# Kernel optimization log

Measured on AMD Instinct MI355X. Metric: run time of the kernel, lower is better.

## Reference

```python
import jax, jax.numpy as jnp
import numpy as np

B, N, K, H = 2, 2048, 48, 128
NIN = 2 * H          # num_in = 2*num_hidden (ProteinMPNN wiring)
FF = 4 * H           # PositionWiseFeedForward hidden
SCALE = 30.0
EPS = 1e-5           # torch LayerNorm default eps


def _ln(x, g, b):
    m = jnp.mean(x, axis=-1, keepdims=True)
    v = jnp.mean((x - m) ** 2, axis=-1, keepdims=True)
    return (x - m) / jnp.sqrt(v + EPS) * g + b


def _gelu(x):
    return jax.nn.gelu(x, approximate=False)  # torch.nn.GELU default (erf)


def _lin(x, W, b):
    return x @ W + b


def setup_inputs() -> dict:
    key = jax.random.key(0)
    ks = jax.random.split(key, 24)
    s = 0.05
    inp = {
        "h_V": jax.random.normal(ks[0], (B, N, H), jnp.float32),
        "h_E": jax.random.normal(ks[1], (B, N, K, H), jnp.float32),
        "E_idx": jax.random.randint(ks[2], (B, N, K), 0, N, jnp.int64),
        "mask_V": jnp.ones((B, N), jnp.float32),
        "mask_attend": jnp.ones((B, N, K), jnp.float32),
        # message MLP (node update): W1 in = H + NIN = 3H
        "W1": jax.random.normal(ks[3], (3 * H, H), jnp.float32) * s,
        "b1": jnp.zeros((H,), jnp.float32),
        "W2": jax.random.normal(ks[4], (H, H), jnp.float32) * s,
        "b2": jnp.zeros((H,), jnp.float32),
        "W3": jax.random.normal(ks[5], (H, H), jnp.float32) * s,
        "b3": jnp.zeros((H,), jnp.float32),
        # PositionWiseFeedForward
        "Wd_in": jax.random.normal(ks[6], (H, FF), jnp.float32) * s,
        "bd_in": jnp.zeros((FF,), jnp.float32),
        "Wd_out": jax.random.normal(ks[7], (FF, H), jnp.float32) * s,
        "bd_out": jnp.zeros((H,), jnp.float32),
        # edge-update MLP: W11 in = H + NIN = 3H
        "W11": jax.random.normal(ks[8], (3 * H, H), jnp.float32) * s,
        "b11": jnp.zeros((H,), jnp.float32),
        "W12": jax.random.normal(ks[9], (H, H), jnp.float32) * s,
        "b12": jnp.zeros((H,), jnp.float32),
        "W13": jax.random.normal(ks[10], (H, H), jnp.float32) * s,
        "b13": jnp.zeros((H,), jnp.float32),
        # LayerNorms
        "n1g": jnp.ones((H,), jnp.float32), "n1b": jnp.zeros((H,), jnp.float32),
        "n2g": jnp.ones((H,), jnp.float32), "n2b": jnp.zeros((H,), jnp.float32),
        "n3g": jnp.ones((H,), jnp.float32), "n3b": jnp.zeros((H,), jnp.float32),
    }
    return inp


def reference(h_V, h_E, E_idx, mask_V, mask_attend,
              W1, b1, W2, b2, W3, b3,
              Wd_in, bd_in, Wd_out, bd_out,
              W11, b11, W12, b12, W13, b13,
              n1g, n1b, n2g, n2b, n3g, n3b):
    gather = jax.vmap(lambda hv, idx: hv[idx])  # [B,N,H],[B,N,K] -> [B,N,K,H]

    # --- node update: cat_neighbors_nodes + expand + 3-layer GELU MLP ---
    h_nb = gather(h_V, E_idx)                                   # [B,N,K,H]
    hV_exp = jnp.broadcast_to(h_V[:, :, None, :], h_nb.shape)   # [B,N,K,H]
    h_EV = jnp.concatenate([hV_exp, h_E, h_nb], axis=-1)        # [B,N,K,3H]
    h_msg = _lin(_gelu(_lin(_gelu(_lin(h_EV, W1, b1)), W2, b2)), W3, b3)
    h_msg = mask_attend[..., None] * h_msg
    dh = jnp.sum(h_msg, axis=-2) / SCALE                        # masked-sum reduce
    h_V = _ln(h_V + dh, n1g, n1b)

    # --- position-wise FFN ---
    dh = _lin(_gelu(_lin(h_V, Wd_in, bd_in)), Wd_out, bd_out)
    h_V = _ln(h_V + dh, n2g, n2b)
    h_V = mask_V[..., None] * h_V

    # --- edge update (not last layer) ---
    h_nb2 = gather(h_V, E_idx)
    hV_exp2 = jnp.broadcast_to(h_V[:, :, None, :], h_nb2.shape)
    h_EV2 = jnp.concatenate([hV_exp2, h_E, h_nb2], axis=-1)     # [B,N,K,3H]
    h_msg2 = _lin(_gelu(_lin(_gelu(_lin(h_EV2, W11, b11)), W12, b12)), W13, b13)
    h_E = _ln(h_E + h_msg2, n3g, n3b)
    return (h_V, h_E)
```

## Files before the change

kernel.cpp:

```cpp
#include <hip/hip_runtime.h>
#include <hip/hip_bf16.h>
#include <stdint.h>

#define XP2 264
#define MP 136
#define FFP 520
#define EPIP 132

typedef __attribute__((ext_vector_type(8))) short bf16x8;
typedef __attribute__((ext_vector_type(4))) float f32x4;

__device__ __forceinline__ f32x4 mfma16(bf16x8 a, bf16x8 b, f32x4 c) {
  return __builtin_amdgcn_mfma_f32_16x16x32_bf16(a, b, c, 0, 0, 0);
}

__device__ __forceinline__ uint16_t f2b(float f) {
  union { __hip_bfloat16 h; uint16_t u; } v;
  v.h = __float2bfloat16(f);
  return v.u;
}
__device__ __forceinline__ uint32_t pk2f(float a, float b) {
  union { __hip_bfloat162 h; uint32_t u; } v;
  v.h = __float22bfloat162_rn(make_float2(a, b));
  return v.u;
}
__device__ __forceinline__ float gelu_f(float x) {
  float u = __builtin_fmaf(x * x, 0.044715f, 1.0f);
  float e = __builtin_amdgcn_exp2f(-2.302585093f * x * u);
  return x * __builtin_amdgcn_rcpf(1.0f + e);
}

__global__ __launch_bounds__(256) void k_prep(
    const float* __restrict__ hV,
    const float* __restrict__ W1, const float* __restrict__ W2, const float* __restrict__ W3,
    const float* __restrict__ WdIn, const float* __restrict__ WdOut,
    const float* __restrict__ W11, const float* __restrict__ W12, const float* __restrict__ W13,
    uint16_t* __restrict__ hVb,
    uint16_t* __restrict__ W1t, uint16_t* __restrict__ W2t, uint16_t* __restrict__ W3t,
    uint16_t* __restrict__ WdInT, uint16_t* __restrict__ WdOutT,
    uint16_t* __restrict__ W11t, uint16_t* __restrict__ W12t, uint16_t* __restrict__ W13t) {
  int i = blockIdx.x * 256 + threadIdx.x;
  if (i < 524288) { hVb[i] = f2b(hV[i]); return; }
  int j = i - 524288;
  if (j < 49152) { int n = j / 384, k = j - n * 384; W1t[j] = f2b(W1[k * 128 + n]); return; }
  j -= 49152;
  if (j < 16384) { int n = j >> 7, k = j & 127; W2t[j] = f2b(W2[k * 128 + n]); return; }
  j -= 16384;
  if (j < 16384) { int n = j >> 7, k = j & 127; W3t[j] = f2b(W3[k * 128 + n]); return; }
  j -= 16384;
  if (j < 65536) { int n = j >> 7, k = j & 127; WdInT[j] = f2b(WdIn[k * 512 + n]); return; }
  j -= 65536;
  if (j < 65536) { int n = j >> 9, k = j & 511; WdOutT[j] = f2b(WdOut[k * 128 + n]); return; }
  j -= 65536;
  if (j < 49152) { int n = j / 384, k = j - n * 384; W11t[j] = f2b(W11[k * 128 + n]); return; }
  j -= 49152;
  if (j < 16384) { int n = j >> 7, k = j & 127; W12t[j] = f2b(W12[k * 128 + n]); return; }
  j -= 16384;
  if (j < 16384) { int n = j >> 7, k = j & 127; W13t[j] = f2b(W13[k * 128 + n]); return; }
}

__global__ __launch_bounds__(256) void k_vec(
    const uint16_t* __restrict__ Xb, const uint16_t* __restrict__ Wt,
    const float* __restrict__ bias, float* __restrict__ C) {
  const int tid = threadIdx.x;
  const int lane = tid & 63, w = tid >> 6, l15 = lane & 15, lg = lane >> 4;
  const int row0 = blockIdx.x * 64 + w * 16;
  f32x4 acc[8] = {};
#pragma unroll
  for (int ks = 0; ks < 4; ++ks) {
    bf16x8 a = *(const bf16x8*)(Xb + (row0 + l15) * 128 + ks * 32 + lg * 8);
#pragma unroll
    for (int j = 0; j < 8; ++j) {
      bf16x8 bb = *(const bf16x8*)(Wt + (j * 16 + l15) * 384 + ks * 32 + lg * 8);
      acc[j] = mfma16(a, bb, acc[j]);
    }
  }
#pragma unroll
  for (int j = 0; j < 8; ++j) {
    float bs = bias[j * 16 + l15];
#pragma unroll
    for (int r = 0; r < 4; ++r)
      C[(row0 + lg * 4 + r) * 128 + j * 16 + l15] = acc[j][r] + bs;
  }
}

#define STAGE_LOAD(TB, GSRC)                                                        \
  do {                                                                              \
    if (cc < 16) {                                                                  \
      _Pragma("unroll") for (int it = 0; it < 6; ++it) {                            \
        const float* s_ = hE + (size_t)((TB) + kr0 + it * 8) * 128 + cc * 8;        \
        sA[it] = *(const float4*)s_;                                                \
        sB[it] = *(const float4*)(s_ + 4);                                          \
      }                                                                             \
    } else {                                                                        \
      _Pragma("unroll") for (int it = 0; it < 6; ++it) {                            \
        int e_ = (TB) + kr0 + it * 8;                                               \
        int nb_ = ((e_ >= 98304) ? 2048 : 0) + eidx[e_];                            \
        *(uint4*)&sA[it] = *(const uint4*)((GSRC) + (size_t)nb_ * 128 + (cc - 16) * 8); \
      }                                                                             \
    }                                                                               \
  } while (0)

#define STAGE_WRITE(BUF)                                                            \
  do {                                                                              \
    if (cc < 16) {                                                                  \
      _Pragma("unroll") for (int it = 0; it < 6; ++it) {                            \
        uint4 v_ = make_uint4(pk2f(sA[it].x, sA[it].y), pk2f(sA[it].z, sA[it].w),   \
                              pk2f(sB[it].x, sB[it].y), pk2f(sB[it].z, sB[it].w));  \
        *(uint4*)((BUF) + (kr0 + it * 8) * XP2 + cc * 8) = v_;                      \
      }                                                                             \
    } else {                                                                        \
      _Pragma("unroll") for (int it = 0; it < 6; ++it)                              \
        *(uint4*)((BUF) + (kr0 + it * 8) * XP2 + cc * 8) = *(uint4*)&sA[it];        \
    }                                                                               \
  } while (0)

#define LAYER256(WT, XSRC, ACC)                                                     \
  do {                                                                              \
    const uint16_t* wr0_ = (WT) + (w * 32 + l15) * 384 + 128 + lg * 8;              \
    const uint16_t* wr1_ = wr0_ + 16 * 384;                                         \
    _Pragma("unroll 2") for (int ks = 0; ks < 8; ++ks) {                            \
      bf16x8 bA_ = *(const bf16x8*)(wr0_ + ks * 32);                                \
      bf16x8 bB_ = *(const bf16x8*)(wr1_ + ks * 32);                                \
      _Pragma("unroll") for (int m = 0; m < 3; ++m) {                               \
        bf16x8 a_ = *(const bf16x8*)((XSRC) + (m * 16 + l15) * XP2 + ks * 32 + lg * 8); \
        ACC[m][0] = mfma16(a_, bA_, ACC[m][0]);                                     \
        ACC[m][1] = mfma16(a_, bB_, ACC[m][1]);                                     \
      }                                                                             \
    }                                                                               \
  } while (0)

#define LAYER128(WT, ASRC, ACC)                                                     \
  do {                                                                              \
    const uint16_t* wr0_ = (WT) + (w * 32 + l15) * 128 + lg * 8;                    \
    const uint16_t* wr1_ = wr0_ + 16 * 128;                                         \
    _Pragma("unroll") for (int ks = 0; ks < 4; ++ks) {                              \
      bf16x8 bA_ = *(const bf16x8*)(wr0_ + ks * 32);                                \
      bf16x8 bB_ = *(const bf16x8*)(wr1_ + ks * 32);                                \
      _Pragma("unroll") for (int m = 0; m < 3; ++m) {                               \
        bf16x8 a_ = *(const bf16x8*)((ASRC) + (m * 16 + l15) * MP + ks * 32 + lg * 8); \
        ACC[m][0] = mfma16(a_, bA_, ACC[m][0]);                                     \
        ACC[m][1] = mfma16(a_, bB_, ACC[m][1]);                                     \
      }                                                                              \
    }                                                                               \
  } while (0)

#define GSTORE(ACC, BIAS, DST)                                                      \
  do {                                                                              \
    float bA_ = (BIAS)[w * 32 + l15];                                               \
    float bB_ = (BIAS)[w * 32 + 16 + l15];                                          \
    _Pragma("unroll") for (int m = 0; m < 3; ++m)                                   \
    _Pragma("unroll") for (int r = 0; r < 4; ++r) {                                 \
      int row_ = m * 16 + lg * 4 + r;                                               \
      (DST)[row_ * MP + w * 32 + l15] = f2b(gelu_f(ACC[m][0][r] + bA_));            \
      (DST)[row_ * MP + w * 32 + 16 + l15] = f2b(gelu_f(ACC[m][1][r] + bB_));       \
    }                                                                               \
  } while (0)

#define GSTORE0(ACC, DST)                                                           \
  do {                                                                              \
    _Pragma("unroll") for (int m = 0; m < 3; ++m)                                   \
    _Pragma("unroll") for (int r = 0; r < 4; ++r) {                                 \
      int row_ = m * 16 + lg * 4 + r;                                               \
      (DST)[row_ * MP + w * 32 + l15] = f2b(gelu_f(ACC[m][0][r]));                  \
      (DST)[row_ * MP + w * 32 + 16 + l15] = f2b(gelu_f(ACC[m][1][r]));             \
    }                                                                               \
  } while (0)

#define ACC_INIT(ACC, CV, ND)                                                       \
  do {                                                                              \
    float c0_ = (CV)[(size_t)(ND) * 128 + w * 32 + l15];                            \
    float c1_ = (CV)[(size_t)(ND) * 128 + w * 32 + 16 + l15];                       \
    _Pragma("unroll") for (int m = 0; m < 3; ++m) {                                 \
      ACC[m][0] = (f32x4){c0_, c0_, c0_, c0_};                                      \
      ACC[m][1] = (f32x4){c1_, c1_, c1_, c1_};                                      \
    }                                                                               \
  } while (0)

__global__ __launch_bounds__(256, 2) void k_node(
    const float* __restrict__ hV, const float* __restrict__ hE,
    const int* __restrict__ eidx, const float* __restrict__ maskA,
    const float* __restrict__ bias2, const float* __restrict__ bias3,
    const float* __restrict__ g1, const float* __restrict__ be1,
    const uint16_t* __restrict__ hVb, const float* __restrict__ C1,
    const uint16_t* __restrict__ W1t, const uint16_t* __restrict__ W2t,
    const uint16_t* __restrict__ W3t,
    float* __restrict__ hV1, uint16_t* __restrict__ hV1b) {
  __shared__ __align__(16) unsigned char lds[76800];
  uint16_t* xtA = (uint16_t*)lds;
  uint16_t* xtB = (uint16_t*)(lds + 25344);
  uint16_t* midA = (uint16_t*)(lds + 50688);
  uint16_t* midB = (uint16_t*)(lds + 63744);
  float* dh = (float*)(lds + 50688);

  const int tid = threadIdx.x;
  const int lane = tid & 63;
  const int w = tid >> 6;
  const int l15 = lane & 15;
  const int lg = lane >> 4;
  const int kr0 = tid >> 5;
  const int cc = tid & 31;

  float4 sA[6], sB[6];
  uint16_t* xc = xtA;
  uint16_t* xn = xtB;

  {
    int tile0 = blockIdx.x;
    STAGE_LOAD(tile0 * 48, hVb);
    STAGE_WRITE(xc);
  }

  for (int t = 0; t < 8; ++t) {
    const int tile = t * 512 + blockIdx.x;
    const int nd = tile;
    const int tbase = tile * 48;
    __syncthreads();

    if (t < 7) STAGE_LOAD((tile + 512) * 48, hVb);

    f32x4 acc1[3][2];
    ACC_INIT(acc1, C1, nd);
    LAYER256(W1t, xc, acc1);
    __syncthreads();
    GSTORE0(acc1, midA);
    __syncthreads();

    f32x4 acc2[3][2] = {};
    LAYER128(W2t, midA, acc2);
    GSTORE(acc2, bias2, midB);
    __syncthreads();

    f32x4 acc3[3][2] = {};
    LAYER128(W3t, midB, acc3);

    if (t < 7) STAGE_WRITE(xn);

    {
      float bA = bias3[w * 32 + l15];
      float bB = bias3[w * 32 + 16 + l15];
      float s0 = 0.f, s1 = 0.f;
#pragma unroll
      for (int m = 0; m < 3; ++m)
#pragma unroll
        for (int r = 0; r < 4; ++r) {
          int row = m * 16 + lg * 4 + r;
          float mk = maskA[tbase + row];
          s0 += (acc3[m][0][r] + bA) * mk;
          s1 += (acc3[m][1][r] + bB) * mk;
        }
      s0 += __shfl_xor(s0, 16); s0 += __shfl_xor(s0, 32);
      s1 += __shfl_xor(s1, 16); s1 += __shfl_xor(s1, 32);
      if (lg == 0) { dh[w * 32 + l15] = s0; dh[w * 32 + 16 + l15] = s1; }
    }
    __syncthreads();

    if (w == 0) {
      const float inv = 1.0f / 30.0f;
      float x0 = hV[(size_t)nd * 128 + lane] + dh[lane] * inv;
      float x1 = hV[(size_t)nd * 128 + 64 + lane] + dh[64 + lane] * inv;
      float s = x0 + x1, q = x0 * x0 + x1 * x1;
#pragma unroll
      for (int off = 1; off < 64; off <<= 1) {
        s += __shfl_xor(s, off);
        q += __shfl_xor(q, off);
      }
      float mean = s * (1.0f / 128.0f);
      float var = q * (1.0f / 128.0f) - mean * mean;
      float rstd = rsqrtf(var + 1e-5f);
      float y0 = (x0 - mean) * rstd * g1[lane] + be1[lane];
      float y1 = (x1 - mean) * rstd * g1[64 + lane] + be1[64 + lane];
      hV1[(size_t)nd * 128 + lane] = y0;
      hV1[(size_t)nd * 128 + 64 + lane] = y1;
      hV1b[(size_t)nd * 128 + lane] = f2b(y0);
      hV1b[(size_t)nd * 128 + 64 + lane] = f2b(y1);
    }

    uint16_t* tmp = xc; xc = xn; xn = tmp;
  }
}

__global__ __launch_bounds__(256, 2) void k_ffn(
    const float* __restrict__ hV1, const uint16_t* __restrict__ hV1b,
    const float* __restrict__ maskV,
    const float* __restrict__ bdin, const float* __restrict__ bdout,
    const float* __restrict__ g2, const float* __restrict__ be2,
    const uint16_t* __restrict__ WdInT, const uint16_t* __restrict__ WdOutT,
    float* __restrict__ outV, uint16_t* __restrict__ hV2b) {
  __shared__ __align__(16) unsigned char lds[20992];
  uint16_t* xa = (uint16_t*)lds;
  uint16_t* mf = (uint16_t*)(lds + 4352);
  float* epi = (float*)(lds + 4352);

  const int tid = threadIdx.x;
  const int lane = tid & 63;
  const int w = tid >> 6;
  const int l15 = lane & 15;
  const int lg = lane >> 4;
  const int node0 = blockIdx.x * 16;

  {
    int row = tid >> 4, c = tid & 15;
    *(uint4*)(xa + row * 136 + (c << 3)) =
        *(const uint4*)(hV1b + (node0 + row) * 128 + (c << 3));
  }
  __syncthreads();

  f32x4 acc[8] = {};
  {
    const uint16_t* ar = xa + l15 * 136 + lg * 8;
#pragma unroll
    for (int ks = 0; ks < 4; ++ks) {
      bf16x8 a = *(const bf16x8*)(ar + ks * 32);
#pragma unroll
      for (int j = 0; j < 8; ++j) {
        bf16x8 bb = *(const bf16x8*)(WdInT + ((w * 8 + j) * 16 + l15) * 128 + ks * 32 + lg * 8);
        acc[j] = mfma16(a, bb, acc[j]);
      }
    }
  }
#pragma unroll
  for (int j = 0; j < 8; ++j) {
    int col = (w * 8 + j) * 16 + l15;
    float bs = bdin[col];
#pragma unroll
    for (int r = 0; r < 4; ++r) {
      int row = lg * 4 + r;
      mf[row * FFP + col] = f2b(gelu_f(acc[j][r] + bs));
    }
  }
  __syncthreads();

  f32x4 acc2[2] = {};
  {
    const uint16_t* mr = mf + l15 * FFP + lg * 8;
#pragma unroll 4
    for (int ks = 0; ks < 16; ++ks) {
      bf16x8 a = *(const bf16x8*)(mr + ks * 32);
#pragma unroll
      for (int t = 0; t < 2; ++t) {
        bf16x8 bb = *(const bf16x8*)(WdOutT + ((w * 2 + t) * 16 + l15) * 512 + ks * 32 + lg * 8);
        acc2[t] = mfma16(a, bb, acc2[t]);
      }
    }
  }
  __syncthreads();
#pragma unroll
  for (int t = 0; t < 2; ++t) {
    int col = (w * 2 + t) * 16 + l15;
    float bs = bdout[col];
#pragma unroll
    for (int r = 0; r < 4; ++r) {
      int row = lg * 4 + r;
      epi[row * EPIP + col] = acc2[t][r] + bs;
    }
  }
  __syncthreads();

#pragma unroll
  for (int rr = 0; rr < 4; ++rr) {
    int row = w * 4 + rr;
    int node = node0 + row;
    float x0 = epi[row * EPIP + lane] + hV1[node * 128 + lane];
    float x1 = epi[row * EPIP + 64 + lane] + hV1[node * 128 + 64 + lane];
    float s = x0 + x1, q = x0 * x0 + x1 * x1;
#pragma unroll
    for (int off = 1; off < 64; off <<= 1) {
      s += __shfl_xor(s, off);
      q += __shfl_xor(q, off);
    }
    float mean = s * (1.0f / 128.0f);
    float var = q * (1.0f / 128.0f) - mean * mean;
    float rstd = rsqrtf(var + 1e-5f);
    float mv = maskV[node];
    float y0 = mv * ((x0 - mean) * rstd * g2[lane] + be2[lane]);
    float y1 = mv * ((x1 - mean) * rstd * g2[64 + lane] + be2[64 + lane]);
    outV[node * 128 + lane] = y0;
    outV[node * 128 + 64 + lane] = y1;
    hV2b[node * 128 + lane] = f2b(y0);
    hV2b[node * 128 + 64 + lane] = f2b(y1);
  }
}

__global__ __launch_bounds__(256, 2) void k_edge(
    const float* __restrict__ hE, const int* __restrict__ eidx,
    const float* __restrict__ bias2, const float* __restrict__ bias3,
    const float* __restrict__ g3, const float* __restrict__ be3,
    const uint16_t* __restrict__ hV2b, const float* __restrict__ C2,
    const uint16_t* __restrict__ W1t, const uint16_t* __restrict__ W2t,
    const uint16_t* __restrict__ W3t,
    float* __restrict__ outE) {
  __shared__ __align__(16) unsigned char lds[76800];
  uint16_t* xtA = (uint16_t*)lds;
  uint16_t* xtB = (uint16_t*)(lds + 25344);
  uint16_t* midA = (uint16_t*)(lds + 50688);
  uint16_t* midB = (uint16_t*)(lds + 63744);
  float* part_s = (float*)(lds + 50688);
  float* part_q = (float*)(lds + 51456);
  float* mstd = (float*)(lds + 52224);

  const int tid = threadIdx.x;
  const int lane = tid & 63;
  const int w = tid >> 6;
  const int l15 = lane & 15;
  const int lg = lane >> 4;
  const int kr0 = tid >> 5;
  const int cc = tid & 31;

  float4 sA[6], sB[6];
  uint16_t* xc = xtA;
  uint16_t* xn = xtB;

  {
    int tile0 = blockIdx.x;
    STAGE_LOAD(tile0 * 48, hV2b);
    STAGE_WRITE(xc);
  }

  for (int t = 0; t < 8; ++t) {
    const int tile = t * 512 + blockIdx.x;
    const int nd = tile;
    const int tbase = tile * 48;
    __syncthreads();

    if (t < 7) STAGE_LOAD((tile + 512) * 48, hV2b);

    f32x4 acc1[3][2];
    ACC_INIT(acc1, C2, nd);
    LAYER256(W1t, xc, acc1);
    __syncthreads();
    GSTORE0(acc1, midA);
    __syncthreads();

    f32x4 acc2[3][2] = {};
    LAYER128(W2t, midA, acc2);
    GSTORE(acc2, bias2, midB);
    __syncthreads();

    f32x4 acc3[3][2] = {};
    LAYER128(W3t, midB, acc3);

    if (t < 7) STAGE_WRITE(xn);

    const float bA = bias3[w * 32 + l15];
    const float bB = bias3[w * 32 + 16 + l15];

    float xs0[3][4], xs1[3][4];
#pragma unroll
    for (int m = 0; m < 3; ++m)
#pragma unroll
      for (int r = 0; r < 4; ++r) {
        int row = m * 16 + lg * 4 + r;
        size_t e = (size_t)tbase + row;
        xs0[m][r] = acc3[m][0][r] + bA + hE[e * 128 + w * 32 + l15];
        xs1[m][r] = acc3[m][1][r] + bB + hE[e * 128 + w * 32 + 16 + l15];
        float s = xs0[m][r] + xs1[m][r];
        float q = xs0[m][r] * xs0[m][r] + xs1[m][r] * xs1[m][r];
        s += __shfl_xor(s, 1); q += __shfl_xor(q, 1);
        s += __shfl_xor(s, 2); q += __shfl_xor(q, 2);
        s += __shfl_xor(s, 4); q += __shfl_xor(q, 4);
        s += __shfl_xor(s, 8); q += __shfl_xor(q, 8);
        if (l15 == 0) { part_s[row * 4 + w] = s; part_q[row * 4 + w] = q; }
      }
    __syncthreads();

    if (tid < 48) {
      float s = part_s[tid * 4] + part_s[tid * 4 + 1] + part_s[tid * 4 + 2] + part_s[tid * 4 + 3];
      float q = part_q[tid * 4] + part_q[tid * 4 + 1] + part_q[tid * 4 + 2] + part_q[tid * 4 + 3];
      float mean = s * (1.0f / 128.0f);
      float var = q * (1.0f / 128.0f) - mean * mean;
      mstd[tid * 2] = mean;
      mstd[tid * 2 + 1] = rsqrtf(var + 1e-5f);
    }
    __syncthreads();

    const float gA = g3[w * 32 + l15], beA = be3[w * 32 + l15];
    const float gB = g3[w * 32 + 16 + l15], beB = be3[w * 32 + 16 + l15];
#pragma unroll
    for (int m = 0; m < 3; ++m)
#pragma unroll
      for (int r = 0; r < 4; ++r) {
        int row = m * 16 + lg * 4 + r;
        size_t e = (size_t)tbase + row;
        float mean = mstd[row * 2];
        float rstd = mstd[row * 2 + 1];
        outE[e * 128 + w * 32 + l15] = (xs0[m][r] - mean) * rstd * gA + beA;
        outE[e * 128 + w * 32 + 16 + l15] = (xs1[m][r] - mean) * rstd * gB + beB;
      }

    uint16_t* tmp = xc; xc = xn; xn = tmp;
  }
}

extern "C" void kernel_launch(void* const* d_in, const int* in_sizes, int n_in,
                              void* d_out, int out_size, void* d_ws, size_t ws_size,
                              hipStream_t stream) {
  const float* hV = (const float*)d_in[0];
  const float* hE = (const float*)d_in[1];
  const int* eidx = (const int*)d_in[2];
  const float* maskV = (const float*)d_in[3];
  const float* maskA = (const float*)d_in[4];
  const float* W1 = (const float*)d_in[5];   const float* b1 = (const float*)d_in[6];
  const float* W2 = (const float*)d_in[7];   const float* b2 = (const float*)d_in[8];
  const float* W3 = (const float*)d_in[9];   const float* b3 = (const float*)d_in[10];
  const float* WdIn = (const float*)d_in[11];  const float* bdin = (const float*)d_in[12];
  const float* WdOut = (const float*)d_in[13]; const float* bdout = (const float*)d_in[14];
  const float* W11 = (const float*)d_in[15]; const float* b11 = (const float*)d_in[16];
  const float* W12 = (const float*)d_in[17]; const float* b12 = (const float*)d_in[18];
  const float* W13 = (const float*)d_in[19]; const float* b13 = (const float*)d_in[20];
  const float* n1g = (const float*)d_in[21]; const float* n1b = (const float*)d_in[22];
  const float* n2g = (const float*)d_in[23]; const float* n2b = (const float*)d_in[24];
  const float* n3g = (const float*)d_in[25]; const float* n3b = (const float*)d_in[26];

  char* ws = (char*)d_ws;
  uint16_t* hVb    = (uint16_t*)(ws + 0);
  uint16_t* W1t    = (uint16_t*)(ws + 1048576);
  uint16_t* W2t    = (uint16_t*)(ws + 1146880);
  uint16_t* W3t    = (uint16_t*)(ws + 1179648);
  uint16_t* WdInT  = (uint16_t*)(ws + 1212416);
  uint16_t* WdOutT = (uint16_t*)(ws + 1343488);
  uint16_t* W11t   = (uint16_t*)(ws + 1474560);
  uint16_t* W12t   = (uint16_t*)(ws + 1572864);
  uint16_t* W13t   = (uint16_t*)(ws + 1605632);
  float*    hV1    = (float*)(ws + 1638400);
  uint16_t* hV1b   = (uint16_t*)(ws + 3735552);
  uint16_t* hV2b   = (uint16_t*)(ws + 4784128);
  float*    C1     = (float*)(ws + 5832704);
  float*    C2     = (float*)(ws + 7929856);

  float* outV = (float*)d_out;
  float* outE = (float*)d_out + 524288;

  k_prep<<<3200, 256, 0, stream>>>(hV, W1, W2, W3, WdIn, WdOut, W11, W12, W13,
                                   hVb, W1t, W2t, W3t, WdInT, WdOutT, W11t, W12t, W13t);
  k_vec<<<64, 256, 0, stream>>>(hVb, W1t, b1, C1);
  k_node<<<512, 256, 0, stream>>>(hV, hE, eidx, maskA, b2, b3, n1g, n1b,
                                  hVb, C1, W1t, W2t, W3t, hV1, hV1b);
  k_ffn<<<256, 256, 0, stream>>>(hV1, hV1b, maskV, bdin, bdout, n2g, n2b,
                                 WdInT, WdOutT, outV, hV2b);
  k_vec<<<64, 256, 0, stream>>>(hV2b, W11t, b11, C2);
  k_edge<<<512, 256, 0, stream>>>(hE, eidx, b12, b13, n3g, n3b,
                                  hV2b, C2, W11t, W12t, W13t, outE);
}
```

Measured before the change: 234.0 us.

## Shrink LDS footprint and retile edge kernel to 32-row tiles for occupancy

Splits the staged input into separate edge and gathered-neighbour LDS buffers and collapses the two mid buffers into one, reusing it with extra barriers, so both kernels use less LDS. The edge kernel moves from 48-row to 32-row tiles with 768 blocks and launch bounds allowing 3 blocks per CU. Because a 32-row tile no longer maps to one node, the per-row node bias is gathered with a divide-by-48 trick. The residual h_E is now read from the bf16 LDS copy instead of fp32 global memory, which saves global traffic but adds bf16 rounding error to the edge output.

```diff
diff --git a/kernel.cpp b/kernel.cpp
--- a/kernel.cpp
+++ b/kernel.cpp
@@ -2,7 +2,6 @@
 #include <hip/hip_bf16.h>
 #include <stdint.h>
 
-#define XP2 264
 #define MP 136
 #define FFP 520
 #define EPIP 132
@@ -19,6 +18,10 @@
   v.h = __float2bfloat16(f);
   return v.u;
 }
+__device__ __forceinline__ float b2f(uint16_t h) {
+  union { uint32_t u; float f; } v; v.u = ((uint32_t)h) << 16;
+  return v.f;
+}
 __device__ __forceinline__ uint32_t pk2f(float a, float b) {
   union { __hip_bfloat162 h; uint32_t u; } v;
   v.h = __float22bfloat162_rn(make_float2(a, b));
@@ -28,6 +31,9 @@
   float u = __builtin_fmaf(x * x, 0.044715f, 1.0f);
   float e = __builtin_amdgcn_exp2f(-2.302585093f * x * u);
   return x * __builtin_amdgcn_rcpf(1.0f + e);
+}
+__device__ __forceinline__ int div48(int e) {
+  return (int)((((unsigned)e >> 4) * 0xAAABu) >> 17);
 }
 
 __global__ __launch_bounds__(256) void k_prep(
@@ -84,60 +90,31 @@
   }
 }
 
-#define STAGE_LOAD(TB, GSRC)                                                        \
-  do {                                                                              \
-    if (cc < 16) {                                                                  \
-      _Pragma("unroll") for (int it = 0; it < 6; ++it) {                            \
-        const float* s_ = hE + (size_t)((TB) + kr0 + it * 8) * 128 + cc * 8;        \
-        sA[it] = *(const float4*)s_;                                                \
-        sB[it] = *(const float4*)(s_ + 4);                                          \
-      }                                                                             \
-    } else {                                                                        \
-      _Pragma("unroll") for (int it = 0; it < 6; ++it) {                            \
-        int e_ = (TB) + kr0 + it * 8;                                               \
-        int nb_ = ((e_ >= 98304) ? 2048 : 0) + eidx[e_];                            \
-        *(uint4*)&sA[it] = *(const uint4*)((GSRC) + (size_t)nb_ * 128 + (cc - 16) * 8); \
-      }                                                                             \
-    }                                                                               \
-  } while (0)
-
-#define STAGE_WRITE(BUF)                                                            \
-  do {                                                                              \
-    if (cc < 16) {                                                                  \
-      _Pragma("unroll") for (int it = 0; it < 6; ++it) {                            \
-        uint4 v_ = make_uint4(pk2f(sA[it].x, sA[it].y), pk2f(sA[it].z, sA[it].w),   \
-                              pk2f(sB[it].x, sB[it].y), pk2f(sB[it].z, sB[it].w));  \
-        *(uint4*)((BUF) + (kr0 + it * 8) * XP2 + cc * 8) = v_;                      \
-      }                                                                             \
-    } else {                                                                        \
-      _Pragma("unroll") for (int it = 0; it < 6; ++it)                              \
-        *(uint4*)((BUF) + (kr0 + it * 8) * XP2 + cc * 8) = *(uint4*)&sA[it];        \
-    }                                                                               \
-  } while (0)
-
-#define LAYER256(WT, XSRC, ACC)                                                     \
+#define LAYER256S(WT, XE, XG, ACC, MM)                                              \
   do {                                                                              \
     const uint16_t* wr0_ = (WT) + (w * 32 + l15) * 384 + 128 + lg * 8;              \
     const uint16_t* wr1_ = wr0_ + 16 * 384;                                         \
-    _Pragma("unroll 2") for (int ks = 0; ks < 8; ++ks) {                            \
+    _Pragma("unroll") for (int ks = 0; ks < 8; ++ks) {                              \
+      const uint16_t* xb_ = (ks < 4) ? (XE) : (XG);                                 \
+      int kk_ = ks & 3;                                                             \
       bf16x8 bA_ = *(const bf16x8*)(wr0_ + ks * 32);                                \
       bf16x8 bB_ = *(const bf16x8*)(wr1_ + ks * 32);                                \
-      _Pragma("unroll") for (int m = 0; m < 3; ++m) {                               \
-        bf16x8 a_ = *(const bf16x8*)((XSRC) + (m * 16 + l15) * XP2 + ks * 32 + lg * 8); \
+      _Pragma("unroll") for (int m = 0; m < (MM); ++m) {                            \
+        bf16x8 a_ = *(const bf16x8*)(xb_ + (m * 16 + l15) * MP + kk_ * 32 + lg * 8);\
         ACC[m][0] = mfma16(a_, bA_, ACC[m][0]);                                     \
         ACC[m][1] = mfma16(a_, bB_, ACC[m][1]);                                     \
       }                                                                             \
     }                                                                               \
   } while (0)
 
-#define LAYER128(WT, ASRC, ACC)                                                     \
+#define LAYER128S(WT, ASRC, ACC, MM)                                                \
   do {                                                                              \
     const uint16_t* wr0_ = (WT) + (w * 32 + l15) * 128 + lg * 8;                    \
     const uint16_t* wr1_ = wr0_ + 16 * 128;                                         \
     _Pragma("unroll") for (int ks = 0; ks < 4; ++ks) {                              \
       bf16x8 bA_ = *(const bf16x8*)(wr0_ + ks * 32);                                \
       bf16x8 bB_ = *(const bf16x8*)(wr1_ + ks * 32);                                \
-      _Pragma("unroll") for (int m = 0; m < 3; ++m) {                               \
+      _Pragma("unroll") for (int m = 0; m < (MM); ++m) {                            \
         bf16x8 a_ = *(const bf16x8*)((ASRC) + (m * 16 + l15) * MP + ks * 32 + lg * 8); \
         ACC[m][0] = mfma16(a_, bA_, ACC[m][0]);                                     \
         ACC[m][1] = mfma16(a_, bB_, ACC[m][1]);                                     \
@@ -145,11 +122,11 @@
     }                                                                               \
   } while (0)
 
-#define GSTORE(ACC, BIAS, DST)                                                      \
+#define GSTOREM(ACC, BIAS, DST, MM)                                                 \
   do {                                                                              \
     float bA_ = (BIAS)[w * 32 + l15];                                               \
     float bB_ = (BIAS)[w * 32 + 16 + l15];                                          \
-    _Pragma("unroll") for (int m = 0; m < 3; ++m)                                   \
+    _Pragma("unroll") for (int m = 0; m < (MM); ++m)                                \
     _Pragma("unroll") for (int r = 0; r < 4; ++r) {                                 \
       int row_ = m * 16 + lg * 4 + r;                                               \
       (DST)[row_ * MP + w * 32 + l15] = f2b(gelu_f(ACC[m][0][r] + bA_));            \
@@ -157,23 +134,13 @@
     }                                                                               \
   } while (0)
 
-#define GSTORE0(ACC, DST)                                                           \
+#define GSTORE0M(ACC, DST, MM)                                                      \
   do {                                                                              \
-    _Pragma("unroll") for (int m = 0; m < 3; ++m)                                   \
+    _Pragma("unroll") for (int m = 0; m < (MM); ++m)                                \
     _Pragma("unroll") for (int r = 0; r < 4; ++r) {                                 \
       int row_ = m * 16 + lg * 4 + r;                                               \
       (DST)[row_ * MP + w * 32 + l15] = f2b(gelu_f(ACC[m][0][r]));                  \
       (DST)[row_ * MP + w * 32 + 16 + l15] = f2b(gelu_f(ACC[m][1][r]));             \
-    }                                                                               \
-  } while (0)
-
-#define ACC_INIT(ACC, CV, ND)                                                       \
-  do {                                                                              \
-    float c0_ = (CV)[(size_t)(ND) * 128 + w * 32 + l15];                            \
-    float c1_ = (CV)[(size_t)(ND) * 128 + w * 32 + 16 + l15];                       \
-    _Pragma("unroll") for (int m = 0; m < 3; ++m) {                                 \
-      ACC[m][0] = (f32x4){c0_, c0_, c0_, c0_};                                      \
-      ACC[m][1] = (f32x4){c1_, c1_, c1_, c1_};                                      \
     }                                                                               \
   } while (0)
 
@@ -186,55 +153,79 @@
     const uint16_t* __restrict__ W1t, const uint16_t* __restrict__ W2t,
     const uint16_t* __restrict__ W3t,
     float* __restrict__ hV1, uint16_t* __restrict__ hV1b) {
-  __shared__ __align__(16) unsigned char lds[76800];
-  uint16_t* xtA = (uint16_t*)lds;
-  uint16_t* xtB = (uint16_t*)(lds + 25344);
-  uint16_t* midA = (uint16_t*)(lds + 50688);
-  uint16_t* midB = (uint16_t*)(lds + 63744);
-  float* dh = (float*)(lds + 50688);
+  __shared__ __align__(16) unsigned char lds[65792];
+  uint16_t* xE0 = (uint16_t*)lds;
+  uint16_t* xE1 = (uint16_t*)(lds + 13056);
+  uint16_t* xG0 = (uint16_t*)(lds + 26112);
+  uint16_t* xG1 = (uint16_t*)(lds + 39168);
+  uint16_t* mid = (uint16_t*)(lds + 52224);
+  float* dh = (float*)(lds + 65280);
 
   const int tid = threadIdx.x;
   const int lane = tid & 63;
   const int w = tid >> 6;
   const int l15 = lane & 15;
   const int lg = lane >> 4;
-  const int kr0 = tid >> 5;
-  const int cc = tid & 31;
-
-  float4 sA[6], sB[6];
-  uint16_t* xc = xtA;
-  uint16_t* xn = xtB;
-
-  {
-    int tile0 = blockIdx.x;
-    STAGE_LOAD(tile0 * 48, hVb);
-    STAGE_WRITE(xc);
-  }
+
+  float4 fE[6];
+  uint4 gV[3];
+
+#define NLOAD48(TB)                                                                 \
+  _Pragma("unroll") for (int i_ = 0; i_ < 3; ++i_) {                                \
+    int c_ = tid + i_ * 256, row_ = c_ >> 4, p_ = c_ & 15;                          \
+    const float* sE_ = hE + (size_t)((TB) + row_) * 128 + p_ * 8;                   \
+    fE[i_ * 2] = *(const float4*)sE_;                                               \
+    fE[i_ * 2 + 1] = *(const float4*)(sE_ + 4);                                     \
+    int e_ = (TB) + row_;                                                           \
+    int nb_ = ((e_ >= 98304) ? 2048 : 0) + eidx[e_];                                \
+    gV[i_] = *(const uint4*)(hVb + (size_t)nb_ * 128 + p_ * 8);                     \
+  }
+
+#define NWRITE48(XE, XG)                                                            \
+  _Pragma("unroll") for (int i_ = 0; i_ < 3; ++i_) {                                \
+    int c_ = tid + i_ * 256, row_ = c_ >> 4, p_ = c_ & 15;                          \
+    uint4 v_ = make_uint4(pk2f(fE[i_ * 2].x, fE[i_ * 2].y),                         \
+                          pk2f(fE[i_ * 2].z, fE[i_ * 2].w),                         \
+                          pk2f(fE[i_ * 2 + 1].x, fE[i_ * 2 + 1].y),                 \
+                          pk2f(fE[i_ * 2 + 1].z, fE[i_ * 2 + 1].w));                \
+    *(uint4*)((XE) + row_ * MP + p_ * 8) = v_;                                      \
+    *(uint4*)((XG) + row_ * MP + p_ * 8) = gV[i_];                                  \
+  }
+
+  uint16_t *xEc = xE0, *xEn = xE1, *xGc = xG0, *xGn = xG1;
+
+  NLOAD48(blockIdx.x * 48);
+  NWRITE48(xEc, xGc);
+  __syncthreads();
 
   for (int t = 0; t < 8; ++t) {
     const int tile = t * 512 + blockIdx.x;
-    const int nd = tile;
     const int tbase = tile * 48;
-    __syncthreads();
-
-    if (t < 7) STAGE_LOAD((tile + 512) * 48, hVb);
+    if (t < 7) NLOAD48((tile + 512) * 48);
 
     f32x4 acc1[3][2];
-    ACC_INIT(acc1, C1, nd);
-    LAYER256(W1t, xc, acc1);
-    __syncthreads();
-    GSTORE0(acc1, midA);
+    {
+      float c0 = C1[(size_t)tile * 128 + w * 32 + l15];
+      float c1 = C1[(size_t)tile * 128 + w * 32 + 16 + l15];
+#pragma unroll
+      for (int m = 0; m < 3; ++m) {
+        acc1[m][0] = (f32x4){c0, c0, c0, c0};
+        acc1[m][1] = (f32x4){c1, c1, c1, c1};
+      }
+    }
+    LAYER256S(W1t, xEc, xGc, acc1, 3);
+    GSTORE0M(acc1, mid, 3);
     __syncthreads();
 
     f32x4 acc2[3][2] = {};
-    LAYER128(W2t, midA, acc2);
-    GSTORE(acc2, bias2, midB);
+    LAYER128S(W2t, mid, acc2, 3);
+    __syncthreads();
+    GSTOREM(acc2, bias2, mid, 3);
     __syncthreads();
 
     f32x4 acc3[3][2] = {};
-    LAYER128(W3t, midB, acc3);
-
-    if (t < 7) STAGE_WRITE(xn);
+    LAYER128S(W3t, mid, acc3, 3);
+    if (t < 7) NWRITE48(xEn, xGn);
 
     {
       float bA = bias3[w * 32 + l15];
@@ -257,8 +248,8 @@
 
     if (w == 0) {
       const float inv = 1.0f / 30.0f;
-      float x0 = hV[(size_t)nd * 128 + lane] + dh[lane] * inv;
-      float x1 = hV[(size_t)nd * 128 + 64 + lane] + dh[64 + lane] * inv;
+      float x0 = hV[(size_t)tile * 128 + lane] + dh[lane] * inv;
+      float x1 = hV[(size_t)tile * 128 + 64 + lane] + dh[64 + lane] * inv;
       float s = x0 + x1, q = x0 * x0 + x1 * x1;
 #pragma unroll
       for (int off = 1; off < 64; off <<= 1) {
@@ -270,14 +261,19 @@
       float rstd = rsqrtf(var + 1e-5f);
       float y0 = (x0 - mean) * rstd * g1[lane] + be1[lane];
       float y1 = (x1 - mean) * rstd * g1[64 + lane] + be1[64 + lane];
-      hV1[(size_t)nd * 128 + lane] = y0;
-      hV1[(size_t)nd * 128 + 64 + lane] = y1;
-      hV1b[(size_t)nd * 128 + lane] = f2b(y0);
-      hV1b[(size_t)nd * 128 + 64 + lane] = f2b(y1);
-    }
-
-    uint16_t* tmp = xc; xc = xn; xn = tmp;
-  }
+      hV1[(size_t)tile * 128 + lane] = y0;
+      hV1[(size_t)tile * 128 + 64 + lane] = y1;
+      hV1b[(size_t)tile * 128 + lane] = f2b(y0);
+      hV1b[(size_t)tile * 128 + 64 + lane] = f2b(y1);
+    }
+    __syncthreads();
+
+    uint16_t* tp;
+    tp = xEc; xEc = xEn; xEn = tp;
+    tp = xGc; xGc = xGn; xGn = tp;
+  }
+#undef NLOAD48
+#undef NWRITE48
 }
 
 __global__ __launch_bounds__(256, 2) void k_ffn(
@@ -382,7 +378,7 @@
   }
 }
 
-__global__ __launch_bounds__(256, 2) void k_edge(
+__global__ __launch_bounds__(256, 3) void k_edge(
     const float* __restrict__ hE, const int* __restrict__ eidx,
     const float* __restrict__ bias2, const float* __restrict__ bias3,
     const float* __restrict__ g3, const float* __restrict__ be3,
@@ -390,70 +386,98 @@
     const uint16_t* __restrict__ W1t, const uint16_t* __restrict__ W2t,
     const uint16_t* __restrict__ W3t,
     float* __restrict__ outE) {
-  __shared__ __align__(16) unsigned char lds[76800];
-  uint16_t* xtA = (uint16_t*)lds;
-  uint16_t* xtB = (uint16_t*)(lds + 25344);
-  uint16_t* midA = (uint16_t*)(lds + 50688);
-  uint16_t* midB = (uint16_t*)(lds + 63744);
-  float* part_s = (float*)(lds + 50688);
-  float* part_q = (float*)(lds + 51456);
-  float* mstd = (float*)(lds + 52224);
+  __shared__ __align__(16) unsigned char lds[44800];
+  uint16_t* xE0 = (uint16_t*)lds;
+  uint16_t* xE1 = (uint16_t*)(lds + 8704);
+  uint16_t* xG0 = (uint16_t*)(lds + 17408);
+  uint16_t* xG1 = (uint16_t*)(lds + 26112);
+  uint16_t* mid = (uint16_t*)(lds + 34816);
+  float* part_s = (float*)(lds + 43520);
+  float* part_q = (float*)(lds + 44032);
+  float* mstd = (float*)(lds + 44544);
 
   const int tid = threadIdx.x;
   const int lane = tid & 63;
   const int w = tid >> 6;
   const int l15 = lane & 15;
   const int lg = lane >> 4;
-  const int kr0 = tid >> 5;
-  const int cc = tid & 31;
-
-  float4 sA[6], sB[6];
-  uint16_t* xc = xtA;
-  uint16_t* xn = xtB;
-
-  {
-    int tile0 = blockIdx.x;
-    STAGE_LOAD(tile0 * 48, hV2b);
-    STAGE_WRITE(xc);
-  }
+
+  float4 fA0, fA1, fA2, fA3;
+  uint4 gA0, gA1;
+
+#define ELOAD32(TB)                                                                 \
+  {                                                                                 \
+    int row_ = tid >> 3, p_ = tid & 7;                                              \
+    const float* sE_ = hE + (size_t)((TB) + row_) * 128 + p_ * 16;                  \
+    fA0 = *(const float4*)sE_;       fA1 = *(const float4*)(sE_ + 4);               \
+    fA2 = *(const float4*)(sE_ + 8); fA3 = *(const float4*)(sE_ + 12);              \
+    int e_ = (TB) + row_;                                                           \
+    int nb_ = ((e_ >= 98304) ? 2048 : 0) + eidx[e_];                                \
+    const uint16_t* sG_ = hV2b + (size_t)nb_ * 128 + p_ * 16;                       \
+    gA0 = *(const uint4*)sG_;  gA1 = *(const uint4*)(sG_ + 8);                      \
+  }
+
+#define EWRITE32(XE, XG)                                                            \
+  {                                                                                 \
+    int row_ = tid >> 3, p_ = tid & 7;                                              \
+    uint4 v0_ = make_uint4(pk2f(fA0.x, fA0.y), pk2f(fA0.z, fA0.w),                  \
+                           pk2f(fA1.x, fA1.y), pk2f(fA1.z, fA1.w));                 \
+    uint4 v1_ = make_uint4(pk2f(fA2.x, fA2.y), pk2f(fA2.z, fA2.w),                  \
+                           pk2f(fA3.x, fA3.y), pk2f(fA3.z, fA3.w));                 \
+    *(uint4*)((XE) + row_ * MP + p_ * 16) = v0_;                                    \
+    *(uint4*)((XE) + row_ * MP + p_ * 16 + 8) = v1_;                                \
+    *(uint4*)((XG) + row_ * MP + p_ * 16) = gA0;                                    \
+    *(uint4*)((XG) + row_ * MP + p_ * 16 + 8) = gA1;                                \
+  }
+
+  uint16_t *xEc = xE0, *xEn = xE1, *xGc = xG0, *xGn = xG1;
+
+  ELOAD32(blockIdx.x * 32);
+  EWRITE32(xEc, xGc);
+  __syncthreads();
 
   for (int t = 0; t < 8; ++t) {
-    const int tile = t * 512 + blockIdx.x;
-    const int nd = tile;
-    const int tbase = tile * 48;
-    __syncthreads();
-
-    if (t < 7) STAGE_LOAD((tile + 512) * 48, hV2b);
-
-    f32x4 acc1[3][2];
-    ACC_INIT(acc1, C2, nd);
-    LAYER256(W1t, xc, acc1);
-    __syncthreads();
-    GSTORE0(acc1, midA);
-    __syncthreads();
-
-    f32x4 acc2[3][2] = {};
-    LAYER128(W2t, midA, acc2);
-    GSTORE(acc2, bias2, midB);
-    __syncthreads();
-
-    f32x4 acc3[3][2] = {};
-    LAYER128(W3t, midB, acc3);
-
-    if (t < 7) STAGE_WRITE(xn);
+    const int tile = t * 768 + blockIdx.x;
+    const int tbase = tile * 32;
+    if (t < 7) ELOAD32((tile + 768) * 32);
+
+    f32x4 acc1[2][2];
+#pragma unroll
+    for (int m = 0; m < 2; ++m)
+#pragma unroll
+      for (int r = 0; r < 4; ++r) {
+        int row = m * 16 + lg * 4 + r;
+        int nd = div48(tbase + row);
+        acc1[m][0][r] = C2[(size_t)nd * 128 + w * 32 + l15];
+        acc1[m][1][r] = C2[(size_t)nd * 128 + w * 32 + 16 + l15];
+      }
+    LAYER256S(W1t, xEc, xGc, acc1, 2);
+    GSTORE0M(acc1, mid, 2);
+    __syncthreads();
+
+    f32x4 acc2[2][2] = {};
+    LAYER128S(W2t, mid, acc2, 2);
+    __syncthreads();
+    GSTOREM(acc2, bias2, mid, 2);
+    __syncthreads();
+
+    f32x4 acc3[2][2] = {};
+    LAYER128S(W3t, mid, acc3, 2);
+    if (t < 7) EWRITE32(xEn, xGn);
 
     const float bA = bias3[w * 32 + l15];
     const float bB = bias3[w * 32 + 16 + l15];
 
-    float xs0[3][4], xs1[3][4];
-#pragma unroll
-    for (int m = 0; m < 3; ++m)
+    float xs0[2][4], xs1[2][4];
+#pragma unroll
+    for (int m = 0; m < 2; ++m)
 #pragma unroll
       for (int r = 0; r < 4; ++r) {
         int row = m * 16 + lg * 4 + r;
-        size_t e = (size_t)tbase + row;
-        xs0[m][r] = acc3[m][0][r] + bA + hE[e * 128 + w * 32 + l15];
-        xs1[m][r] = acc3[m][1][r] + bB + hE[e * 128 + w * 32 + 16 + l15];
+        float r0 = b2f(xEc[row * MP + w * 32 + l15]);
+        float r1 = b2f(xEc[row * MP + w * 32 + 16 + l15]);
+        xs0[m][r] = acc3[m][0][r] + bA + r0;
+        xs1[m][r] = acc3[m][1][r] + bB + r1;
         float s = xs0[m][r] + xs1[m][r];
         float q = xs0[m][r] * xs0[m][r] + xs1[m][r] * xs1[m][r];
         s += __shfl_xor(s, 1); q += __shfl_xor(q, 1);
@@ -464,7 +488,7 @@
       }
     __syncthreads();
 
-    if (tid < 48) {
+    if (tid < 32) {
       float s = part_s[tid * 4] + part_s[tid * 4 + 1] + part_s[tid * 4 + 2] + part_s[tid * 4 + 3];
       float q = part_q[tid * 4] + part_q[tid * 4 + 1] + part_q[tid * 4 + 2] + part_q[tid * 4 + 3];
       float mean = s * (1.0f / 128.0f);
@@ -477,7 +501,7 @@
     const float gA = g3[w * 32 + l15], beA = be3[w * 32 + l15];
     const float gB = g3[w * 32 + 16 + l15], beB = be3[w * 32 + 16 + l15];
 #pragma unroll
-    for (int m = 0; m < 3; ++m)
+    for (int m = 0; m < 2; ++m)
 #pragma unroll
       for (int r = 0; r < 4; ++r) {
         int row = m * 16 + lg * 4 + r;
@@ -487,9 +511,14 @@
         outE[e * 128 + w * 32 + l15] = (xs0[m][r] - mean) * rstd * gA + beA;
         outE[e * 128 + w * 32 + 16 + l15] = (xs1[m][r] - mean) * rstd * gB + beB;
       }
-
-    uint16_t* tmp = xc; xc = xn; xn = tmp;
-  }
+    __syncthreads();
+
+    uint16_t* tp;
+    tp = xEc; xEc = xEn; xEn = tp;
+    tp = xGc; xGc = xGn; xGn = tp;
+  }
+#undef ELOAD32
+#undef EWRITE32
 }
 
 extern "C" void kernel_launch(void* const* d_in, const int* in_sizes, int n_in,
@@ -539,6 +568,6 @@
   k_ffn<<<256, 256, 0, stream>>>(hV1, hV1b, maskV, bdin, bdout, n2g, n2b,
                                  WdInT, WdOutT, outV, hV2b);
   k_vec<<<64, 256, 0, stream>>>(hV2b, W11t, b11, C2);
-  k_edge<<<512, 256, 0, stream>>>(hE, eidx, b12, b13, n3g, n3b,
+  k_edge<<<768, 256, 0, stream>>>(hE, eidx, b12, b13, n3g, n3b,
                                   hV2b, C2, W11t, W12t, W13t, outE);
 }
```

Result: slower. 289.9 us (+23.9%).
